# Kernel tuning notes

Hardware: AMD Instinct MI355X
Metric: run time of the kernel (lower is better)

Reference implementation:

```python
import jax, jax.numpy as jnp
import numpy as np

B, S, D = 4, 4096, 1024

def setup_inputs() -> dict:
    key = jax.random.key(0)
    k1, k2 = jax.random.split(key)
    x = jax.random.normal(k1, (B, S, D), dtype=jnp.float32)
    W_qkv = jax.random.normal(k2, (D, 3 * D), dtype=jnp.float32) * (D ** -0.5)
    b_qkv = jnp.zeros((3 * D,), dtype=jnp.float32)
    return {"x": x, "W_qkv": W_qkv, "b_qkv": b_qkv}

def reference(x, W_qkv, b_qkv):
    # qkv projection: [B,S,3D]
    qkv = jnp.einsum('bsd,de->bse', x, W_qkv) + b_qkv
    q, k, v = jnp.split(qkv, 3, axis=-1)  # each [B,S,D]
    scale = q.shape[-1] ** -0.5
    # full [B,S,S] score matrix, as in the original (non-fused) implementation
    scores = jnp.einsum('bqd,bkd->bqk', q, k) * scale
    attn = jax.nn.softmax(scores, axis=-1)
    out = jnp.einsum('bqk,bkd->bqd', attn, v)
    return out
```

## Files before the change

kernel.cpp:

```cpp
#include <hip/hip_runtime.h>
#include <math.h>

typedef unsigned short ushort_t;
typedef __attribute__((ext_vector_type(8))) short short8;
typedef __attribute__((ext_vector_type(4))) float floatx4;

#define VMCNT(n) asm volatile("s_waitcnt vmcnt(" #n ")" ::: "memory")

__device__ inline ushort_t f2bf(float x) {
    union { float f; unsigned int u; } c; c.f = x;
    unsigned int r = (c.u + 0x7fffu + ((c.u >> 16) & 1u)) >> 16;
    return (ushort_t)r;
}

__device__ __forceinline__ void glds16(const ushort_t* g, ushort_t* l) {
    __builtin_amdgcn_global_load_lds(
        (const __attribute__((address_space(1))) unsigned int*)g,
        (__attribute__((address_space(3))) unsigned int*)l,
        16, 0, 0);
}

__device__ __forceinline__ unsigned swzo(unsigned off) {
    return off ^ ((off >> 3) & 0x70u);
}

__global__ __launch_bounds__(256)
void wt_kernel(const float* __restrict__ W, ushort_t* __restrict__ Wt)
{
    __shared__ float tile[64][65];
    const int k0 = blockIdx.x * 64;
    const int n0 = blockIdx.y * 64;
    const int tid = threadIdx.x;
    #pragma unroll
    for (int ii = 0; ii < 16; ++ii) {
        int idx = ii * 256 + tid;
        int r = idx >> 6, c = idx & 63;
        tile[r][c] = W[(size_t)(k0 + r) * 3072 + n0 + c];
    }
    __syncthreads();
    #pragma unroll
    for (int ii = 0; ii < 16; ++ii) {
        int idx = ii * 256 + tid;
        int r = idx >> 6, c = idx & 63;
        Wt[(size_t)(n0 + r) * 1024 + k0 + c] = f2bf(tile[c][r]);
    }
}

__global__ __launch_bounds__(256)
void xcvt(const float* __restrict__ x, ushort_t* __restrict__ xb)
{
    const int i = (blockIdx.x * 256 + threadIdx.x) * 8;
    float4 f0 = *(const float4*)(x + i);
    float4 f1 = *(const float4*)(x + i + 4);
    ushort_t tmp[8] __attribute__((aligned(16)));
    tmp[0]=f2bf(f0.x); tmp[1]=f2bf(f0.y); tmp[2]=f2bf(f0.z); tmp[3]=f2bf(f0.w);
    tmp[4]=f2bf(f1.x); tmp[5]=f2bf(f1.y); tmp[6]=f2bf(f1.z); tmp[7]=f2bf(f1.w);
    *(uint4*)(xb + i) = *(const uint4*)tmp;
}

__global__ __launch_bounds__(256)
void qkv_mfma(const float* __restrict__ x, const ushort_t* __restrict__ Wt,
              const float* __restrict__ bias,
              ushort_t* __restrict__ q, ushort_t* __restrict__ k,
              ushort_t* __restrict__ vt)
{
    __shared__ ushort_t As[128][72];
    __shared__ ushort_t Bs[128][72];
    const int tid = threadIdx.x;
    const int w = tid >> 6, lane = tid & 63;
    const int m = lane & 15, quad = lane >> 4;
    const int col0 = blockIdx.x * 128;
    const int r0   = blockIdx.y * 128;

    floatx4 o[2][8];
    #pragma unroll
    for (int rf = 0; rf < 2; ++rf)
        #pragma unroll
        for (int nf = 0; nf < 8; ++nf)
            o[rf][nf] = (floatx4){0.f, 0.f, 0.f, 0.f};

    for (int kc = 0; kc < 16; ++kc) {
        const int kdim = kc * 64;
        __syncthreads();
        #pragma unroll
        for (int ii = 0; ii < 4; ++ii) {
            int lin = ii * 256 + tid;
            int row = lin >> 3, seg = lin & 7;
            const float* src = x + (size_t)(r0 + row) * 1024 + kdim + seg * 8;
            float4 f0 = *(const float4*)src;
            float4 f1 = *(const float4*)(src + 4);
            ushort_t tmp[8] __attribute__((aligned(16)));
            tmp[0]=f2bf(f0.x); tmp[1]=f2bf(f0.y); tmp[2]=f2bf(f0.z); tmp[3]=f2bf(f0.w);
            tmp[4]=f2bf(f1.x); tmp[5]=f2bf(f1.y); tmp[6]=f2bf(f1.z); tmp[7]=f2bf(f1.w);
            *(uint4*)&As[row][seg * 8] = *(const uint4*)tmp;
        }
        #pragma unroll
        for (int ii = 0; ii < 4; ++ii) {
            int lin = ii * 256 + tid;
            int row = lin >> 3, seg = lin & 7;
            const ushort_t* src = Wt + (size_t)(col0 + row) * 1024 + kdim + seg * 8;
            *(uint4*)&Bs[row][seg * 8] = *(const uint4*)src;
        }
        __syncthreads();
        #pragma unroll
        for (int kk = 0; kk < 2; ++kk) {
            short8 af[2];
            #pragma unroll
            for (int rf = 0; rf < 2; ++rf)
                af[rf] = *(const short8*)&As[w * 32 + rf * 16 + m][kk * 32 + quad * 8];
            #pragma unroll
            for (int nf = 0; nf < 8; ++nf) {
                short8 bf = *(const short8*)&Bs[nf * 16 + m][kk * 32 + quad * 8];
                #pragma unroll
                for (int rf = 0; rf < 2; ++rf)
                    o[rf][nf] = __builtin_amdgcn_mfma_f32_16x16x32_bf16(af[rf], bf, o[rf][nf], 0, 0, 0);
            }
        }
    }

    const int which = col0 >> 10;
    const int dbase = col0 & 1023;
    float bias_v[8];
    #pragma unroll
    for (int nf = 0; nf < 8; ++nf) bias_v[nf] = bias[col0 + nf * 16 + m];

    #pragma unroll
    for (int rf = 0; rf < 2; ++rf) {
        #pragma unroll
        for (int e = 0; e < 4; ++e) {
            const int g = r0 + w * 32 + rf * 16 + quad * 4 + e;
            #pragma unroll
            for (int nf = 0; nf < 8; ++nf) {
                const int c = dbase + nf * 16 + m;
                float val = o[rf][nf][e] + bias_v[nf];
                if (which == 0) {
                    q[(size_t)g * 1024 + c] = f2bf(val * 0.03125f);
                } else if (which == 1) {
                    k[(size_t)g * 1024 + c] = f2bf(val);
                } else {
                    vt[(size_t)(g >> 12) * 4194304 + (size_t)c * 4096 + (g & 4095)] = f2bf(val);
                }
            }
        }
    }
}

__global__ __launch_bounds__(256)
void qkv_mfma2(const ushort_t* __restrict__ xb, const ushort_t* __restrict__ Wt,
               const float* __restrict__ bias,
               ushort_t* __restrict__ q, ushort_t* __restrict__ k,
               ushort_t* __restrict__ vt)
{
    __shared__ __align__(1024) ushort_t As[128][64];
    __shared__ __align__(1024) ushort_t Bs[128][64];
    const int tid = threadIdx.x;
    const int w = tid >> 6, lane = tid & 63;
    const int m = lane & 15, quad = lane >> 4;
    const int lx = lane ^ ((lane >> 3) & 7);
    const int sr = lx >> 3, sc = (lx & 7) * 8;
    const int col0 = blockIdx.x * 128;
    const int r0   = blockIdx.y * 128;

    floatx4 o[2][8];
    #pragma unroll
    for (int rf = 0; rf < 2; ++rf)
        #pragma unroll
        for (int nf = 0; nf < 8; ++nf)
            o[rf][nf] = (floatx4){0.f, 0.f, 0.f, 0.f};

    for (int kc = 0; kc < 16; ++kc) {
        const int kdim = kc * 64;
        __syncthreads();
        #pragma unroll
        for (int ii = 0; ii < 4; ++ii) {
            glds16(xb + (size_t)(r0 + w * 32 + ii * 8 + sr) * 1024 + kdim + sc,
                   &As[w * 32 + ii * 8][0]);
            glds16(Wt + (size_t)(col0 + w * 32 + ii * 8 + sr) * 1024 + kdim + sc,
                   &Bs[w * 32 + ii * 8][0]);
        }
        __syncthreads();
        #pragma unroll
        for (int kk = 0; kk < 2; ++kk) {
            short8 af[2];
            #pragma unroll
            for (int rf = 0; rf < 2; ++rf)
                af[rf] = *(const short8*)((const char*)As +
                          swzo((unsigned)((w * 32 + rf * 16 + m) * 128 + kk * 64 + quad * 16)));
            #pragma unroll
            for (int nf = 0; nf < 8; ++nf) {
                short8 bf = *(const short8*)((const char*)Bs +
                          swzo((unsigned)((nf * 16 + m) * 128 + kk * 64 + quad * 16)));
                #pragma unroll
                for (int rf = 0; rf < 2; ++rf)
                    o[rf][nf] = __builtin_amdgcn_mfma_f32_16x16x32_bf16(af[rf], bf, o[rf][nf], 0, 0, 0);
            }
        }
    }

    const int which = col0 >> 10;
    const int dbase = col0 & 1023;
    float bias_v[8];
    #pragma unroll
    for (int nf = 0; nf < 8; ++nf) bias_v[nf] = bias[col0 + nf * 16 + m];

    #pragma unroll
    for (int rf = 0; rf < 2; ++rf) {
        #pragma unroll
        for (int e = 0; e < 4; ++e) {
            const int g = r0 + w * 32 + rf * 16 + quad * 4 + e;
            #pragma unroll
            for (int nf = 0; nf < 8; ++nf) {
                const int c = dbase + nf * 16 + m;
                float val = o[rf][nf][e] + bias_v[nf];
                if (which == 0) {
                    q[(size_t)g * 1024 + c] = f2bf(val * 0.03125f);
                } else if (which == 1) {
                    k[(size_t)g * 1024 + c] = f2bf(val);
                } else {
                    vt[(size_t)(g >> 12) * 4194304 + (size_t)c * 4096 + (g & 4095)] = f2bf(val);
                }
            }
        }
    }
}

__global__ __launch_bounds__(512, 2)
void fused_attn(const ushort_t* __restrict__ q, const ushort_t* __restrict__ kb_,
                const ushort_t* __restrict__ vt, float* __restrict__ out)
{
    __shared__ __align__(1024) unsigned char lds[141312];
    ushort_t (*Qs)[128][32] = (ushort_t(*)[128][32])(lds);
    ushort_t (*Ks)[256][32] = (ushort_t(*)[256][32])(lds + 24576);
    ushort_t (*Pls)[264]    = (ushort_t(*)[264])(lds);
    ushort_t (*Vs)[512][32] = (ushort_t(*)[512][32])(lds + 73728);
    float    (*redL)[4]     = (float(*)[4])(lds + 139264);

    const int tid  = threadIdx.x;
    const int w    = tid >> 6, lane = tid & 63;
    const int m    = lane & 15, quad = lane >> 4;
    const int wr   = w & 1, wc = w >> 1;
    const int lx   = lane ^ ((lane >> 3) & 7);
    const int lr   = lx >> 2, lc = (lx & 3) * 8;
    const int n0x  = blockIdx.x * 512;
    const int r0   = blockIdx.y * 128;
    const int b    = blockIdx.z;
    const size_t qoff = (size_t)b * 4096 * 1024;
    const size_t voff = (size_t)b * 4194304;

    unsigned qof[4], kof[4], vof[8];
    #pragma unroll
    for (int i = 0; i < 4; ++i)
        qof[i] = swzo((unsigned)((wr * 64 + i * 16 + m) * 64 + quad * 16));
    #pragma unroll
    for (int j = 0; j < 4; ++j)
        kof[j] = swzo((unsigned)((wc * 64 + j * 16 + m) * 64 + quad * 16));
    #pragma unroll
    for (int j = 0; j < 8; ++j)
        vof[j] = swzo((unsigned)((wc * 128 + j * 16 + m) * 64 + quad * 16));

    const ushort_t* qsrc  = q   + qoff + (size_t)(r0 + w * 16 + lr) * 1024 + lc;
    const ushort_t* ksrc0 = kb_ + qoff + (size_t)(w * 32 + lr) * 1024 + lc;
    const ushort_t* ksrc1 = kb_ + qoff + (size_t)(w * 32 + 16 + lr) * 1024 + lc;

    floatx4 o[4][8];
    #pragma unroll
    for (int i = 0; i < 4; ++i)
        #pragma unroll
        for (int j = 0; j < 8; ++j)
            o[i][j] = (floatx4){0.f, 0.f, 0.f, 0.f};
    float lsum[4][4] = {};

    for (int kt = 0; kt < 16; ++kt) {
        const int kbase = kt * 256;

        floatx4 s[4][4];
        #pragma unroll
        for (int i = 0; i < 4; ++i)
            #pragma unroll
            for (int j = 0; j < 4; ++j)
                s[i][j] = (floatx4){0.f, 0.f, 0.f, 0.f};

        glds16(qsrc,                        &Qs[0][w * 16][0]);
        glds16(ksrc0 + (size_t)kbase * 1024, &Ks[0][w * 32][0]);
        glds16(ksrc1 + (size_t)kbase * 1024, &Ks[0][w * 32 + 16][0]);
        {
            int cur = 0;
            for (int kc = 0; kc < 32; ++kc) {
                if (kc < 31) {
                    const int nxt = (cur == 2) ? 0 : cur + 1;
                    const int kd = (kc + 1) * 32;
                    glds16(qsrc + kd,                             &Qs[nxt][w * 16][0]);
                    glds16(ksrc0 + (size_t)kbase * 1024 + kd,     &Ks[nxt][w * 32][0]);
                    glds16(ksrc1 + (size_t)kbase * 1024 + kd,     &Ks[nxt][w * 32 + 16][0]);
                    VMCNT(3);
                } else {
                    VMCNT(0);
                }
                __builtin_amdgcn_s_barrier();
                __builtin_amdgcn_sched_barrier(0);
                short8 af[4], bf[4];
                #pragma unroll
                for (int i = 0; i < 4; ++i)
                    af[i] = *(const short8*)((const char*)Qs[cur] + qof[i]);
                #pragma unroll
                for (int j = 0; j < 4; ++j)
                    bf[j] = *(const short8*)((const char*)Ks[cur] + kof[j]);
                __builtin_amdgcn_s_setprio(1);
                #pragma unroll
                for (int i = 0; i < 4; ++i)
                    #pragma unroll
                    for (int j = 0; j < 4; ++j)
                        s[i][j] = __builtin_amdgcn_mfma_f32_16x16x32_bf16(af[i], bf[j], s[i][j], 0, 0, 0);
                __builtin_amdgcn_s_setprio(0);
                cur = (cur == 2) ? 0 : cur + 1;
            }
        }
        __syncthreads();

        #pragma unroll
        for (int i = 0; i < 4; ++i)
            #pragma unroll
            for (int j = 0; j < 4; ++j)
                #pragma unroll
                for (int e = 0; e < 4; ++e) {
                    float pv = __expf(s[i][j][e]);
                    lsum[i][e] += pv;
                    Pls[wr * 64 + i * 16 + quad * 4 + e][wc * 64 + j * 16 + m] = f2bf(pv);
                }

        {
            #pragma unroll
            for (int i = 0; i < 4; ++i)
                glds16(vt + voff + (size_t)(n0x + w * 64 + i * 16 + lr) * 4096 + kbase + lc,
                       &Vs[0][w * 64 + i * 16][0]);
        }
        __syncthreads();
        for (int vc = 0; vc < 8; ++vc) {
            const int p = vc & 1;
            if (vc < 7) {
                const int kd = kbase + (vc + 1) * 32;
                #pragma unroll
                for (int i = 0; i < 4; ++i)
                    glds16(vt + voff + (size_t)(n0x + w * 64 + i * 16 + lr) * 4096 + kd + lc,
                           &Vs[p ^ 1][w * 64 + i * 16][0]);
            }
            short8 ap[4], bv[8];
            #pragma unroll
            for (int i = 0; i < 4; ++i)
                ap[i] = *(const short8*)&Pls[wr * 64 + i * 16 + m][vc * 32 + quad * 8];
            #pragma unroll
            for (int j = 0; j < 8; ++j)
                bv[j] = *(const short8*)((const char*)Vs[p] + vof[j]);
            __builtin_amdgcn_s_setprio(1);
            #pragma unroll
            for (int i = 0; i < 4; ++i)
                #pragma unroll
                for (int j = 0; j < 8; ++j)
                    o[i][j] = __builtin_amdgcn_mfma_f32_16x16x32_bf16(ap[i], bv[j], o[i][j], 0, 0, 0);
            __builtin_amdgcn_s_setprio(0);
            __syncthreads();
        }
    }

    #pragma unroll
    for (int i = 0; i < 4; ++i)
        #pragma unroll
        for (int e = 0; e < 4; ++e) {
            float l = lsum[i][e];
            l += __shfl_xor(l, 1);
            l += __shfl_xor(l, 2);
            l += __shfl_xor(l, 4);
            l += __shfl_xor(l, 8);
            if (m == 0) redL[wr * 64 + i * 16 + quad * 4 + e][wc] = l;
        }
    __syncthreads();
    #pragma unroll
    for (int i = 0; i < 4; ++i)
        #pragma unroll
        for (int e = 0; e < 4; ++e) {
            const int row = wr * 64 + i * 16 + quad * 4 + e;
            const float inv = 1.0f / (redL[row][0] + redL[row][1] + redL[row][2] + redL[row][3]);
            const int g = b * 4096 + r0 + row;
            #pragma unroll
            for (int j = 0; j < 8; ++j)
                out[(size_t)g * 1024 + n0x + wc * 128 + j * 16 + m] = o[i][j][e] * inv;
        }
}

extern "C" void kernel_launch(void* const* d_in, const int* in_sizes, int n_in,
                              void* d_out, int out_size, void* d_ws, size_t ws_size,
                              hipStream_t stream)
{
    const float* x    = (const float*)d_in[0];
    const float* W    = (const float*)d_in[1];
    const float* bias = (const float*)d_in[2];
    float* out = (float*)d_out;

    const size_t SZQ  = (size_t)4 * 4096 * 1024 * 2;
    const size_t SZWT = (size_t)3072 * 1024 * 2;
    const size_t SZXB = (size_t)4 * 4096 * 1024 * 2;
    const size_t NEED  = 3 * SZQ + SZWT;
    const size_t NEED2 = NEED + SZXB;
    if (ws_size < NEED) return;

    ushort_t* q  = (ushort_t*)d_ws;
    ushort_t* k  = (ushort_t*)((char*)d_ws + SZQ);
    ushort_t* vt = (ushort_t*)((char*)d_ws + 2 * SZQ);
    ushort_t* Wt = (ushort_t*)((char*)d_ws + 3 * SZQ);
    ushort_t* xb = (ushort_t*)((char*)d_ws + NEED);

    wt_kernel <<<dim3(16, 48),   256, 0, stream>>>(W, Wt);
    if (ws_size >= NEED2) {
        xcvt      <<<dim3(8192),    256, 0, stream>>>(x, xb);
        qkv_mfma2 <<<dim3(24, 128), 256, 0, stream>>>(xb, Wt, bias, q, k, vt);
    } else {
        qkv_mfma  <<<dim3(24, 128), 256, 0, stream>>>(x, Wt, bias, q, k, vt);
    }
    fused_attn<<<dim3(2, 32, 4), 512, 0, stream>>>(q, k, vt, out);
}
```

Before: 756.2 us.

## Stage V-transpose through LDS and triple-buffer attention V loads with swizzled P

The QKV kernel now writes the transposed V output by staging tiles in shared memory and issuing 16-byte coalesced stores, replacing strided 2-byte scattered writes. The attention kernel changes its LDS layout. Q gets its own double buffer loaded after the barrier, and the P tile gets an XOR swizzle to reduce bank conflicts. V loads move to a triple-buffered pipeline with vmcnt waits and plain barriers instead of a full sync each step, and the first V tile is prefetched before the exp/softmax phase. LDS use grows to 160KB, which may change occupancy, and the buffer aliasing adds some correctness risk.

Result: slower. 890.1 us (+17.7%).

```diff
diff --git a/kernel.cpp b/kernel.cpp
--- a/kernel.cpp
+++ b/kernel.cpp
@@ -151,8 +151,9 @@
                ushort_t* __restrict__ q, ushort_t* __restrict__ k,
                ushort_t* __restrict__ vt)
 {
-    __shared__ __align__(1024) ushort_t As[128][64];
-    __shared__ __align__(1024) ushort_t Bs[128][64];
+    __shared__ __align__(1024) ushort_t smem[2 * 128 * 64];
+    ushort_t (*As)[64] = (ushort_t (*)[64])smem;
+    ushort_t (*Bs)[64] = (ushort_t (*)[64])(smem + 128 * 64);
     const int tid = threadIdx.x;
     const int w = tid >> 6, lane = tid & 63;
     const int m = lane & 15, quad = lane >> 4;
@@ -203,21 +204,48 @@
     #pragma unroll
     for (int nf = 0; nf < 8; ++nf) bias_v[nf] = bias[col0 + nf * 16 + m];
 
-    #pragma unroll
-    for (int rf = 0; rf < 2; ++rf) {
-        #pragma unroll
-        for (int e = 0; e < 4; ++e) {
-            const int g = r0 + w * 32 + rf * 16 + quad * 4 + e;
-            #pragma unroll
-            for (int nf = 0; nf < 8; ++nf) {
-                const int c = dbase + nf * 16 + m;
-                float val = o[rf][nf][e] + bias_v[nf];
-                if (which == 0) {
-                    q[(size_t)g * 1024 + c] = f2bf(val * 0.03125f);
-                } else if (which == 1) {
-                    k[(size_t)g * 1024 + c] = f2bf(val);
-                } else {
-                    vt[(size_t)(g >> 12) * 4194304 + (size_t)c * 4096 + (g & 4095)] = f2bf(val);
+    if (which == 2) {
+        const size_t voffb = (size_t)(r0 >> 12) * 4194304;
+        const int grow0 = r0 & 4095;
+        ushort_t (*T)[136] = (ushort_t (*)[136])smem;
+        #pragma unroll
+        for (int p = 0; p < 2; ++p) {
+            __syncthreads();
+            #pragma unroll
+            for (int rf = 0; rf < 2; ++rf)
+                #pragma unroll
+                for (int e = 0; e < 4; ++e) {
+                    const int row = w * 32 + rf * 16 + quad * 4 + e;
+                    #pragma unroll
+                    for (int nn = 0; nn < 4; ++nn) {
+                        const int nf = p * 4 + nn;
+                        T[nn * 16 + m][row] = f2bf(o[rf][nf][e] + bias_v[nf]);
+                    }
+                }
+            __syncthreads();
+            #pragma unroll
+            for (int ii = 0; ii < 4; ++ii) {
+                int idx = ii * 256 + tid;
+                int c = idx >> 4, seg = idx & 15;
+                *(uint4*)&vt[voffb + (size_t)(dbase + p * 64 + c) * 4096 + grow0 + seg * 8]
+                    = *(const uint4*)&T[c][seg * 8];
+            }
+        }
+    } else {
+        #pragma unroll
+        for (int rf = 0; rf < 2; ++rf) {
+            #pragma unroll
+            for (int e = 0; e < 4; ++e) {
+                const int g = r0 + w * 32 + rf * 16 + quad * 4 + e;
+                #pragma unroll
+                for (int nf = 0; nf < 8; ++nf) {
+                    const int c = dbase + nf * 16 + m;
+                    float val = o[rf][nf][e] + bias_v[nf];
+                    if (which == 0) {
+                        q[(size_t)g * 1024 + c] = f2bf(val * 0.03125f);
+                    } else {
+                        k[(size_t)g * 1024 + c] = f2bf(val);
+                    }
                 }
             }
         }
@@ -228,12 +256,11 @@
 void fused_attn(const ushort_t* __restrict__ q, const ushort_t* __restrict__ kb_,
                 const ushort_t* __restrict__ vt, float* __restrict__ out)
 {
-    __shared__ __align__(1024) unsigned char lds[141312];
+    __shared__ __align__(1024) unsigned char lds[163840];
     ushort_t (*Qs)[128][32] = (ushort_t(*)[128][32])(lds);
-    ushort_t (*Ks)[256][32] = (ushort_t(*)[256][32])(lds + 24576);
-    ushort_t (*Pls)[264]    = (ushort_t(*)[264])(lds);
-    ushort_t (*Vs)[512][32] = (ushort_t(*)[512][32])(lds + 73728);
-    float    (*redL)[4]     = (float(*)[4])(lds + 139264);
+    ushort_t (*Ks)[256][32] = (ushort_t(*)[256][32])(lds + 16384);
+    ushort_t (*Vs)[512][32] = (ushort_t(*)[512][32])(lds + 65536);
+    float    (*redL)[4]     = (float(*)[4])(lds);
 
     const int tid  = threadIdx.x;
     const int w    = tid >> 6, lane = tid & 63;
@@ -258,6 +285,14 @@
     for (int j = 0; j < 8; ++j)
         vof[j] = swzo((unsigned)((wc * 128 + j * 16 + m) * 64 + quad * 16));
 
+    unsigned pbase[4], pflip[4];
+    #pragma unroll
+    for (int i = 0; i < 4; ++i) {
+        const int prow = wr * 64 + i * 16 + m;
+        pbase[i] = ((unsigned)prow << 9) + (((unsigned)quad << 4) ^ (((unsigned)(prow & 3)) << 4));
+        pflip[i] = ((unsigned)((prow >> 2) & 1)) << 6;
+    }
+
     const ushort_t* qsrc  = q   + qoff + (size_t)(r0 + w * 16 + lr) * 1024 + lc;
     const ushort_t* ksrc0 = kb_ + qoff + (size_t)(w * 32 + lr) * 1024 + lc;
     const ushort_t* ksrc1 = kb_ + qoff + (size_t)(w * 32 + 16 + lr) * 1024 + lc;
@@ -280,31 +315,33 @@
             for (int j = 0; j < 4; ++j)
                 s[i][j] = (floatx4){0.f, 0.f, 0.f, 0.f};
 
-        glds16(qsrc,                        &Qs[0][w * 16][0]);
         glds16(ksrc0 + (size_t)kbase * 1024, &Ks[0][w * 32][0]);
         glds16(ksrc1 + (size_t)kbase * 1024, &Ks[0][w * 32 + 16][0]);
+        glds16(qsrc,                         &Qs[0][w * 16][0]);
         {
-            int cur = 0;
+            int curK = 0;
             for (int kc = 0; kc < 32; ++kc) {
+                const int nxtK = (curK == 2) ? 0 : curK + 1;
                 if (kc < 31) {
-                    const int nxt = (cur == 2) ? 0 : cur + 1;
                     const int kd = (kc + 1) * 32;
-                    glds16(qsrc + kd,                             &Qs[nxt][w * 16][0]);
-                    glds16(ksrc0 + (size_t)kbase * 1024 + kd,     &Ks[nxt][w * 32][0]);
-                    glds16(ksrc1 + (size_t)kbase * 1024 + kd,     &Ks[nxt][w * 32 + 16][0]);
-                    VMCNT(3);
+                    glds16(ksrc0 + (size_t)kbase * 1024 + kd, &Ks[nxtK][w * 32][0]);
+                    glds16(ksrc1 + (size_t)kbase * 1024 + kd, &Ks[nxtK][w * 32 + 16][0]);
+                    VMCNT(2);
                 } else {
                     VMCNT(0);
                 }
                 __builtin_amdgcn_s_barrier();
                 __builtin_amdgcn_sched_barrier(0);
+                if (kc < 31) {
+                    glds16(qsrc + (kc + 1) * 32, &Qs[(kc + 1) & 1][w * 16][0]);
+                }
                 short8 af[4], bf[4];
                 #pragma unroll
                 for (int i = 0; i < 4; ++i)
-                    af[i] = *(const short8*)((const char*)Qs[cur] + qof[i]);
+                    af[i] = *(const short8*)((const char*)Qs[kc & 1] + qof[i]);
                 #pragma unroll
                 for (int j = 0; j < 4; ++j)
-                    bf[j] = *(const short8*)((const char*)Ks[cur] + kof[j]);
+                    bf[j] = *(const short8*)((const char*)Ks[curK] + kof[j]);
                 __builtin_amdgcn_s_setprio(1);
                 #pragma unroll
                 for (int i = 0; i < 4; ++i)
@@ -312,10 +349,15 @@
                     for (int j = 0; j < 4; ++j)
                         s[i][j] = __builtin_amdgcn_mfma_f32_16x16x32_bf16(af[i], bf[j], s[i][j], 0, 0, 0);
                 __builtin_amdgcn_s_setprio(0);
-                cur = (cur == 2) ? 0 : cur + 1;
-            }
-        }
-        __syncthreads();
+                curK = nxtK;
+            }
+        }
+        __syncthreads();
+
+        #pragma unroll
+        for (int i = 0; i < 4; ++i)
+            glds16(vt + voff + (size_t)(n0x + w * 64 + i * 16 + lr) * 4096 + kbase + lc,
+                   &Vs[0][w * 64 + i * 16][0]);
 
         #pragma unroll
         for (int i = 0; i < 4; ++i)
@@ -325,41 +367,47 @@
                 for (int e = 0; e < 4; ++e) {
                     float pv = __expf(s[i][j][e]);
                     lsum[i][e] += pv;
-                    Pls[wr * 64 + i * 16 + quad * 4 + e][wc * 64 + j * 16 + m] = f2bf(pv);
-                }
+                    const int prow = wr * 64 + i * 16 + quad * 4 + e;
+                    const unsigned pcolb = (unsigned)((wc * 64 + j * 16 + m) << 1);
+                    *(ushort_t*)(lds + ((unsigned)prow << 9) +
+                                 (pcolb ^ (((unsigned)(prow & 7)) << 4))) = f2bf(pv);
+                }
+        __syncthreads();
 
         {
-            #pragma unroll
-            for (int i = 0; i < 4; ++i)
-                glds16(vt + voff + (size_t)(n0x + w * 64 + i * 16 + lr) * 4096 + kbase + lc,
-                       &Vs[0][w * 64 + i * 16][0]);
-        }
-        __syncthreads();
-        for (int vc = 0; vc < 8; ++vc) {
-            const int p = vc & 1;
-            if (vc < 7) {
-                const int kd = kbase + (vc + 1) * 32;
+            int curV = 0;
+            for (int vc = 0; vc < 8; ++vc) {
+                const int nxtV = (curV == 2) ? 0 : curV + 1;
+                if (vc < 7) {
+                    const int kd = kbase + (vc + 1) * 32;
+                    #pragma unroll
+                    for (int i = 0; i < 4; ++i)
+                        glds16(vt + voff + (size_t)(n0x + w * 64 + i * 16 + lr) * 4096 + kd + lc,
+                               &Vs[nxtV][w * 64 + i * 16][0]);
+                    VMCNT(4);
+                } else {
+                    VMCNT(0);
+                }
+                __builtin_amdgcn_s_barrier();
+                __builtin_amdgcn_sched_barrier(0);
+                short8 ap[4], bv[8];
                 #pragma unroll
                 for (int i = 0; i < 4; ++i)
-                    glds16(vt + voff + (size_t)(n0x + w * 64 + i * 16 + lr) * 4096 + kd + lc,
-                           &Vs[p ^ 1][w * 64 + i * 16][0]);
-            }
-            short8 ap[4], bv[8];
-            #pragma unroll
-            for (int i = 0; i < 4; ++i)
-                ap[i] = *(const short8*)&Pls[wr * 64 + i * 16 + m][vc * 32 + quad * 8];
-            #pragma unroll
-            for (int j = 0; j < 8; ++j)
-                bv[j] = *(const short8*)((const char*)Vs[p] + vof[j]);
-            __builtin_amdgcn_s_setprio(1);
-            #pragma unroll
-            for (int i = 0; i < 4; ++i)
+                    ap[i] = *(const short8*)(lds + pbase[i] + (((unsigned)vc << 6) ^ pflip[i]));
                 #pragma unroll
                 for (int j = 0; j < 8; ++j)
-                    o[i][j] = __builtin_amdgcn_mfma_f32_16x16x32_bf16(ap[i], bv[j], o[i][j], 0, 0, 0);
-            __builtin_amdgcn_s_setprio(0);
-            __syncthreads();
-        }
+                    bv[j] = *(const short8*)((const char*)Vs[curV] + vof[j]);
+                __builtin_amdgcn_s_setprio(1);
+                #pragma unroll
+                for (int i = 0; i < 4; ++i)
+                    #pragma unroll
+                    for (int j = 0; j < 8; ++j)
+                        o[i][j] = __builtin_amdgcn_mfma_f32_16x16x32_bf16(ap[i], bv[j], o[i][j], 0, 0, 0);
+                __builtin_amdgcn_s_setprio(0);
+                curV = nxtV;
+            }
+        }
+        __syncthreads();
     }
 
     #pragma unroll
```
